# Kernel tuning notes

Hardware: AMD Instinct MI355X
Metric: run time of the kernel (lower is better)

The kernel has to match this reference:

```python
import jax, jax.numpy as jnp
import numpy as np

N_NODES = 100000
N_EDGES = 1200000
N_GRAPHS = 512
F_IN = 7
H = 64
N_CLASSES = 10


def _xavier(key, shape):
    fan_in, fan_out = shape[0], shape[1]
    limit = float(np.sqrt(6.0 / (fan_in + fan_out)))
    return jax.random.uniform(key, shape, jnp.float32, -limit, limit)


def setup_inputs() -> dict:
    key = jax.random.key(0)
    ks = jax.random.split(key, 16)
    x = jax.random.normal(ks[0], (N_NODES, F_IN), jnp.float32)
    edge_index = jax.random.randint(ks[1], (2, N_EDGES), 0, N_NODES, jnp.int64)
    batch = jnp.sort(jax.random.randint(ks[2], (N_NODES,), 0, N_GRAPHS, jnp.int64))
    d = {
        'x': x, 'edge_index': edge_index, 'batch': batch,
        'W_emb': _xavier(ks[3], (F_IN, H)), 'b_emb': jnp.zeros((H,), jnp.float32),
        'eps1': jnp.zeros((), jnp.float32),
        'W1a': _xavier(ks[4], (H, 2 * H)), 'b1a': jnp.zeros((2 * H,), jnp.float32),
        'W1b': _xavier(ks[5], (2 * H, H)), 'b1b': jnp.zeros((H,), jnp.float32),
        'eps2': jnp.zeros((), jnp.float32),
        'W2a': _xavier(ks[6], (H, 2 * H)), 'b2a': jnp.zeros((2 * H,), jnp.float32),
        'W2b': _xavier(ks[7], (2 * H, H)), 'b2b': jnp.zeros((H,), jnp.float32),
        'eps3': jnp.zeros((), jnp.float32),
        'W3a': _xavier(ks[8], (H, 2 * H)), 'b3a': jnp.zeros((2 * H,), jnp.float32),
        'W3b': _xavier(ks[9], (2 * H, H)), 'b3b': jnp.zeros((H,), jnp.float32),
        'Wc1': _xavier(ks[10], (2 * H, H)), 'bc1': jnp.zeros((H,), jnp.float32),
        'Wc2': _xavier(ks[11], (H, N_CLASSES)), 'bc2': jnp.zeros((N_CLASSES,), jnp.float32),
    }
    return d


def _gin_layer(x, eps, Wa, ba, Wb, bb, src, dst):
    # scatter-add aggregation of source features into destination nodes
    agg = jax.ops.segment_sum(x[src], dst, num_segments=N_NODES)
    h = (1.0 + eps) * x + agg
    h = jax.nn.relu(h @ Wa + ba) @ Wb + bb
    return jax.nn.elu(h)  # dropout is identity in eval mode


def reference(x, edge_index, batch,
              W_emb, b_emb,
              eps1, W1a, b1a, W1b, b1b,
              eps2, W2a, b2a, W2b, b2b,
              eps3, W3a, b3a, W3b, b3b,
              Wc1, bc1, Wc2, bc2):
    src, dst = edge_index[0], edge_index[1]
    h = x @ W_emb + b_emb                      # [N, H]
    h = _gin_layer(h, eps1, W1a, b1a, W1b, b1b, src, dst)
    h = _gin_layer(h, eps2, W2a, b2a, W2b, b2b, src, dst)
    h = _gin_layer(h, eps3, W3a, b3a, W3b, b3b, src, dst)
    # global mean + max pool per graph
    sums = jax.ops.segment_sum(h, batch, num_segments=N_GRAPHS)
    cnts = jax.ops.segment_sum(jnp.ones((h.shape[0], 1), h.dtype), batch, num_segments=N_GRAPHS)
    mean = sums / jnp.maximum(cnts, 1.0)
    mx = jax.ops.segment_max(h, batch, num_segments=N_GRAPHS)
    g = jnp.concatenate([mean, mx], axis=1)    # [G, 2H]
    out = jax.nn.relu(g @ Wc1 + bc1) @ Wc2 + bc2
    return out
```

## Files before the change

### kernel.cpp

```cpp
#include <hip/hip_runtime.h>
#include <hip/hip_bf16.h>
#include <math.h>

#define N_NODES 100000
#define N_EDGES 1200000
#define N_GRAPHS 512
#define NBUCKET 196
#define BSHIFT 9
#define TILE 2048
#define CSR_CAP 8192

typedef __bf16 bf16x8 __attribute__((ext_vector_type(8)));
typedef float f32x4 __attribute__((ext_vector_type(4)));

__device__ __forceinline__ unsigned f2ord(float f) {
  unsigned u = __float_as_uint(f);
  return (u & 0x80000000u) ? ~u : (u | 0x80000000u);
}
__device__ __forceinline__ float ord2f(unsigned u) {
  return (u & 0x80000000u) ? __uint_as_float(u & 0x7fffffffu) : __uint_as_float(~u);
}
__device__ __forceinline__ float bflo(unsigned u) { return __uint_as_float(u << 16); }
__device__ __forceinline__ float bfhi(unsigned u) { return __uint_as_float(u & 0xFFFF0000u); }

__global__ void bucket_hist_kernel(const int* __restrict__ dst, int* __restrict__ bcnt) {
  __shared__ int c[256];
  int t = threadIdx.x;
  c[t] = 0;
  __syncthreads();
  for (int e = blockIdx.x * 256 + t; e < N_EDGES; e += gridDim.x * 256)
    atomicAdd(&c[dst[e] >> BSHIFT], 1);
  __syncthreads();
  if (t < NBUCKET && c[t] > 0) atomicAdd(&bcnt[t], c[t]);
}

__global__ void bucket_scan_kernel(const int* __restrict__ bcnt,
                                   int* __restrict__ bbase,
                                   int* __restrict__ bcursor,
                                   int* __restrict__ rowp) {
  __shared__ int s[256];
  int t = threadIdx.x;
  int own = (t < NBUCKET) ? bcnt[t] : 0;
  s[t] = own;
  __syncthreads();
  for (int o = 1; o < 256; o <<= 1) {
    int v = (t >= o) ? s[t - o] : 0;
    __syncthreads();
    s[t] += v;
    __syncthreads();
  }
  if (t < NBUCKET) {
    int excl = s[t] - own;
    bbase[t] = excl;
    bcursor[t] = excl;
  }
  if (t == 0) {
    bbase[NBUCKET] = N_EDGES;
    rowp[N_NODES] = N_EDGES;
  }
}

__global__ void partition_kernel(const int* __restrict__ src, const int* __restrict__ dst,
                                 int* __restrict__ bcursor, unsigned* __restrict__ ent) {
  __shared__ int cnt[256];
  __shared__ int cnt2[256];
  __shared__ int lstart[256];
  __shared__ int gbase[256];
  __shared__ int s[256];
  __shared__ unsigned sorted[TILE];
  __shared__ unsigned char bid[TILE];
  int t = threadIdx.x;
  int e0 = blockIdx.x * TILE;
  cnt[t] = 0; cnt2[t] = 0;
  __syncthreads();

  unsigned v[8];
  int b[8];
#pragma unroll
  for (int u = 0; u < 8; ++u) {
    int e = e0 + u * 256 + t;
    b[u] = -1;
    if (e < N_EDGES) {
      int d = dst[e];
      b[u] = d >> BSHIFT;
      v[u] = (unsigned)src[e] | ((unsigned)(d & 511) << 17);
      atomicAdd(&cnt[b[u]], 1);
    }
  }
  __syncthreads();
  s[t] = cnt[t];
  __syncthreads();
  for (int o = 1; o < 256; o <<= 1) {
    int x = (t >= o) ? s[t - o] : 0;
    __syncthreads();
    s[t] += x;
    __syncthreads();
  }
  lstart[t] = s[t] - cnt[t];
  __syncthreads();
  if (t < NBUCKET) gbase[t] = (cnt[t] > 0) ? atomicAdd(&bcursor[t], cnt[t]) : 0;
  __syncthreads();
#pragma unroll
  for (int u = 0; u < 8; ++u) {
    if (b[u] >= 0) {
      int p = lstart[b[u]] + atomicAdd(&cnt2[b[u]], 1);
      sorted[p] = v[u];
      bid[p] = (unsigned char)b[u];
    }
  }
  __syncthreads();
  int ntile = min(TILE, N_EDGES - e0);
  for (int i = t; i < ntile; i += 256) {
    int bb = bid[i];
    ent[gbase[bb] + (i - lstart[bb])] = sorted[i];
  }
}

__launch_bounds__(256)
__global__ void bucket_csr_kernel(const unsigned* __restrict__ ent,
                                  const int* __restrict__ bbase,
                                  int* __restrict__ rowp,
                                  int* __restrict__ ssrc) {
  __shared__ unsigned le[CSR_CAP];
  __shared__ int deg[512];
  __shared__ int excl[512];
  __shared__ int ws[256];
  int t = threadIdx.x;
  int b = blockIdx.x;
  int base = bbase[b];
  int cntb = bbase[b + 1] - base;
  deg[t] = 0; deg[t + 256] = 0;
  __syncthreads();
  for (int i = t; i < cntb; i += 256) {
    unsigned e = ent[base + i];
    if (i < CSR_CAP) le[i] = e;
    atomicAdd(&deg[e >> 17], 1);
  }
  __syncthreads();
  int d0 = deg[t * 2], d1 = deg[t * 2 + 1];
  int sum2 = d0 + d1;
  ws[t] = sum2;
  __syncthreads();
  for (int o = 1; o < 256; o <<= 1) {
    int x = (t >= o) ? ws[t - o] : 0;
    __syncthreads();
    ws[t] += x;
    __syncthreads();
  }
  int run = ws[t] - sum2;
  excl[t * 2] = run; run += d0;
  excl[t * 2 + 1] = run;
  __syncthreads();
  int node0 = b << BSHIFT;
#pragma unroll
  for (int k = 0; k < 2; ++k) {
    int i = t * 2 + k;
    int n = node0 + i;
    if (n < N_NODES) rowp[n] = base + excl[i];
    deg[i] = excl[i];
  }
  __syncthreads();
  for (int i = t; i < cntb; i += 256) {
    unsigned e = (i < CSR_CAP) ? le[i] : ent[base + i];
    int p = atomicAdd(&deg[e >> 17], 1);
    ssrc[base + p] = (int)(e & 0x1FFFFu);
  }
}

__global__ void embed_kernel(const float* __restrict__ x,
                             const float* __restrict__ W,
                             const float* __restrict__ b,
                             __bf16* __restrict__ h) {
  __shared__ float Ws[7 * 64];
  __shared__ float bs[64];
  int t = threadIdx.x;
  for (int i = t; i < 7 * 64; i += 256) Ws[i] = W[i];
  if (t < 64) bs[t] = b[t];
  __syncthreads();
  int gid = blockIdx.x * 256 + t;
  int n = gid >> 6, f = gid & 63;
  const float* xr = x + n * 7;
  float acc = bs[f];
#pragma unroll
  for (int k = 0; k < 7; ++k) acc = fmaf(xr[k], Ws[k * 64 + f], acc);
  h[gid] = (__bf16)acc;
}

__global__ void convert_all_kernel(const float* __restrict__ W1a, const float* __restrict__ W1b,
                                   const float* __restrict__ W2a, const float* __restrict__ W2b,
                                   const float* __restrict__ W3a, const float* __restrict__ W3b,
                                   __bf16* __restrict__ wp,
                                   float* gsum, unsigned* gmax, int* gcnt) {
  int o = blockIdx.x * 256 + threadIdx.x;
  if (o < N_GRAPHS * 64) {
    gsum[o] = 0.0f;
    gmax[o] = 0x407FFFFFu;
  }
  if (o < N_GRAPHS) gcnt[o] = 0;
  int L = o >> 14, q = o & 16383;
  const float* Wa = (L == 0) ? W1a : (L == 1) ? W2a : W3a;
  const float* Wb = (L == 0) ? W1b : (L == 1) ? W2b : W3b;
  if (q < 8192) {
    int j = q & 7, c = (q >> 3) & 15, kc = (q >> 7) & 3, kt = (q >> 9) & 1, nt = q >> 10;
    wp[o] = (__bf16)Wa[(kt * 32 + kc * 8 + j) * 128 + nt * 16 + c];
  } else {
    int p = q - 8192;
    int j = p & 7, c = (p >> 3) & 15, kc = (p >> 7) & 3, kt = (p >> 9) & 3, nt2 = p >> 11;
    wp[o] = (__bf16)Wb[(kt * 32 + kc * 8 + j) * 64 + nt2 * 16 + c];
  }
}

__launch_bounds__(256)
__global__ void gin_fused4_kernel(const __bf16* __restrict__ hin,
                                  __bf16* __restrict__ hout,
                                  const int* __restrict__ row_ptr,
                                  const int* __restrict__ ssrc,
                                  const float* __restrict__ eps_p,
                                  const __bf16* __restrict__ W1p,
                                  const float* __restrict__ b1,
                                  const __bf16* __restrict__ W2p,
                                  const float* __restrict__ b2) {
  __shared__ __bf16 SM[4 * 2176];
  int t = threadIdx.x, lane = t & 63, wv = t >> 6;
  int c = lane & 15, kc = lane >> 4;
  int hl2 = (lane & 31) * 2;
  int par = lane >> 5;
  __bf16* AsW = &SM[wv * 2176];
  __bf16* HsW = AsW;
  float epsv = 1.0f + eps_p[0];
  int n0b = blockIdx.x * 64;
  int n0w = n0b + wv * 16;

  int rp = row_ptr[min(n0w + min(lane, 16), N_NODES)];

#define LD2(sidx) (*(const unsigned*)&hin[(size_t)(sidx) * 64 + hl2])

  for (int rr = 0; rr < 8; ++rr) {
    int rA = rr, rB = rr + 8;
    int nA = n0w + rA, nB = n0w + rB;
    int jA = __builtin_amdgcn_readfirstlane(__shfl(rp, rA));
    int eA = __builtin_amdgcn_readfirstlane(__shfl(rp, rA + 1));
    int jB = __builtin_amdgcn_readfirstlane(__shfl(rp, rB));
    int eB = __builtin_amdgcn_readfirstlane(__shfl(rp, rB + 1));
    float axA = 0.f, ayA = 0.f, axB = 0.f, ayB = 0.f;
    if (par == 0) {
      if (nA < N_NODES) { unsigned u = LD2(nA); axA = epsv * bflo(u); ayA = epsv * bfhi(u); }
      if (nB < N_NODES) { unsigned u = LD2(nB); axB = epsv * bflo(u); ayB = epsv * bfhi(u); }
    }
    while (jA + 8 <= eA && jB + 8 <= eB) {
      int a0 = ssrc[jA], a1 = ssrc[jA+1], a2 = ssrc[jA+2], a3 = ssrc[jA+3];
      int a4 = ssrc[jA+4], a5 = ssrc[jA+5], a6 = ssrc[jA+6], a7 = ssrc[jA+7];
      int b0 = ssrc[jB], b1_ = ssrc[jB+1], b2_ = ssrc[jB+2], b3_ = ssrc[jB+3];
      int b4 = ssrc[jB+4], b5 = ssrc[jB+5], b6 = ssrc[jB+6], b7 = ssrc[jB+7];
      unsigned uA0 = LD2(par ? a1 : a0), uA1 = LD2(par ? a3 : a2);
      unsigned uA2 = LD2(par ? a5 : a4), uA3 = LD2(par ? a7 : a6);
      unsigned uB0 = LD2(par ? b1_ : b0), uB1 = LD2(par ? b3_ : b2_);
      unsigned uB2 = LD2(par ? b5 : b4), uB3 = LD2(par ? b7 : b6);
      axA += (bflo(uA0) + bflo(uA1)) + (bflo(uA2) + bflo(uA3));
      ayA += (bfhi(uA0) + bfhi(uA1)) + (bfhi(uA2) + bfhi(uA3));
      axB += (bflo(uB0) + bflo(uB1)) + (bflo(uB2) + bflo(uB3));
      ayB += (bfhi(uB0) + bfhi(uB1)) + (bfhi(uB2) + bfhi(uB3));
      jA += 8; jB += 8;
    }
    while (jA + 8 <= eA) {
      int a0 = ssrc[jA], a1 = ssrc[jA+1], a2 = ssrc[jA+2], a3 = ssrc[jA+3];
      int a4 = ssrc[jA+4], a5 = ssrc[jA+5], a6 = ssrc[jA+6], a7 = ssrc[jA+7];
      unsigned u0 = LD2(par ? a1 : a0), u1 = LD2(par ? a3 : a2);
      unsigned u2 = LD2(par ? a5 : a4), u3 = LD2(par ? a7 : a6);
      axA += (bflo(u0) + bflo(u1)) + (bflo(u2) + bflo(u3));
      ayA += (bfhi(u0) + bfhi(u1)) + (bfhi(u2) + bfhi(u3));
      jA += 8;
    }
    if (jA + 4 <= eA) {
      int a0 = ssrc[jA], a1 = ssrc[jA+1], a2 = ssrc[jA+2], a3 = ssrc[jA+3];
      unsigned u0 = LD2(par ? a1 : a0), u1 = LD2(par ? a3 : a2);
      axA += bflo(u0) + bflo(u1);
      ayA += bfhi(u0) + bfhi(u1);
      jA += 4;
    }
    if (jA + 2 <= eA) {
      int a0 = ssrc[jA], a1 = ssrc[jA+1];
      unsigned u0 = LD2(par ? a1 : a0);
      axA += bflo(u0); ayA += bfhi(u0);
      jA += 2;
    }
    if (jA < eA && par == 0) {
      unsigned u0 = LD2(ssrc[jA]);
      axA += bflo(u0); ayA += bfhi(u0);
    }
    while (jB + 8 <= eB) {
      int b0 = ssrc[jB], b1_ = ssrc[jB+1], b2_ = ssrc[jB+2], b3_ = ssrc[jB+3];
      int b4 = ssrc[jB+4], b5 = ssrc[jB+5], b6 = ssrc[jB+6], b7 = ssrc[jB+7];
      unsigned u0 = LD2(par ? b1_ : b0), u1 = LD2(par ? b3_ : b2_);
      unsigned u2 = LD2(par ? b5 : b4), u3 = LD2(par ? b7 : b6);
      axB += (bflo(u0) + bflo(u1)) + (bflo(u2) + bflo(u3));
      ayB += (bfhi(u0) + bfhi(u1)) + (bfhi(u2) + bfhi(u3));
      jB += 8;
    }
    if (jB + 4 <= eB) {
      int b0 = ssrc[jB], b1_ = ssrc[jB+1], b2_ = ssrc[jB+2], b3_ = ssrc[jB+3];
      unsigned u0 = LD2(par ? b1_ : b0), u1 = LD2(par ? b3_ : b2_);
      axB += bflo(u0) + bflo(u1);
      ayB += bfhi(u0) + bfhi(u1);
      jB += 4;
    }
    if (jB + 2 <= eB) {
      int b0 = ssrc[jB], b1_ = ssrc[jB+1];
      unsigned u0 = LD2(par ? b1_ : b0);
      axB += bflo(u0); ayB += bfhi(u0);
      jB += 2;
    }
    if (jB < eB && par == 0) {
      unsigned u0 = LD2(ssrc[jB]);
      axB += bflo(u0); ayB += bfhi(u0);
    }
    axA += __shfl_xor(axA, 32); ayA += __shfl_xor(ayA, 32);
    axB += __shfl_xor(axB, 32); ayB += __shfl_xor(ayB, 32);
    if (par == 0) {
      union { __bf16 b[2]; unsigned u; } pA, pB;
      pA.b[0] = (__bf16)axA; pA.b[1] = (__bf16)ayA;
      pB.b[0] = (__bf16)axB; pB.b[1] = (__bf16)ayB;
      *(unsigned*)&AsW[rA * 72 + hl2] = pA.u;
      *(unsigned*)&AsW[rB * 72 + hl2] = pB.u;
    }
  }
#undef LD2

  bf16x8 a1_0 = *(const bf16x8*)&AsW[c * 72 + 0 * 32 + kc * 8];
  bf16x8 a1_1 = *(const bf16x8*)&AsW[c * 72 + 1 * 32 + kc * 8];
  f32x4 acc1[8];
#pragma unroll
  for (int nt = 0; nt < 8; ++nt) {
    float bv = b1[nt * 16 + c];
    f32x4 acc = {bv, bv, bv, bv};
    bf16x8 bf0 = *(const bf16x8*)&W1p[(nt * 2 + 0) * 512 + kc * 128 + c * 8];
    bf16x8 bf1 = *(const bf16x8*)&W1p[(nt * 2 + 1) * 512 + kc * 128 + c * 8];
    acc = __builtin_amdgcn_mfma_f32_16x16x32_bf16(a1_0, bf0, acc, 0, 0, 0);
    acc = __builtin_amdgcn_mfma_f32_16x16x32_bf16(a1_1, bf1, acc, 0, 0, 0);
    acc1[nt] = acc;
  }
#pragma unroll
  for (int nt = 0; nt < 8; ++nt) {
#pragma unroll
    for (int r = 0; r < 4; ++r) {
      HsW[(kc * 4 + r) * 136 + nt * 16 + c] = (__bf16)fmaxf(acc1[nt][r], 0.0f);
    }
  }

  bf16x8 a2[4];
#pragma unroll
  for (int kt = 0; kt < 4; ++kt)
    a2[kt] = *(const bf16x8*)&HsW[c * 136 + kt * 32 + kc * 8];
#pragma unroll
  for (int nt2 = 0; nt2 < 4; ++nt2) {
    float bv = b2[nt2 * 16 + c];
    f32x4 acc = {bv, bv, bv, bv};
#pragma unroll
    for (int kt = 0; kt < 4; ++kt) {
      bf16x8 bf = *(const bf16x8*)&W2p[(nt2 * 4 + kt) * 512 + kc * 128 + c * 8];
      acc = __builtin_amdgcn_mfma_f32_16x16x32_bf16(a2[kt], bf, acc, 0, 0, 0);
    }
#pragma unroll
    for (int r = 0; r < 4; ++r) {
      int g = n0b + wv * 16 + kc * 4 + r;
      if (g < N_NODES) {
        float o = acc[r];
        hout[(size_t)g * 64 + nt2 * 16 + c] = (__bf16)((o > 0.0f) ? o : expm1f(o));
      }
    }
  }
}

__global__ void pool_kernel(const __bf16* __restrict__ h,
                            const int* __restrict__ batch,
                            float* gsum, unsigned* gmax, int* gcnt) {
  int lane = threadIdx.x & 63;
  int wave = (blockIdx.x * blockDim.x + threadIdx.x) >> 6;
  int nwaves = (gridDim.x * blockDim.x) >> 6;
  int chunk = (N_NODES + nwaves - 1) / nwaves;
  int n0 = wave * chunk;
  int n1 = min(n0 + chunk, N_NODES);
  if (n0 >= N_NODES) return;
  int cur = batch[n0];
  float s = 0.0f, m = -2.0f;
  int cnt = 0;
  for (int n = n0; n < n1; ++n) {
    int g = batch[n];
    if (g != cur) {
      atomicAdd(&gsum[cur * 64 + lane], s);
      atomicMax(&gmax[cur * 64 + lane], f2ord(m));
      if (lane == 0) atomicAdd(&gcnt[cur], cnt);
      cur = g; s = 0.0f; m = -2.0f; cnt = 0;
    }
    float v = (float)h[(size_t)n * 64 + lane];
    s += v;
    m = fmaxf(m, v);
    ++cnt;
  }
  atomicAdd(&gsum[cur * 64 + lane], s);
  atomicMax(&gmax[cur * 64 + lane], f2ord(m));
  if (lane == 0) atomicAdd(&gcnt[cur], cnt);
}

__global__ void cls_kernel(const float* __restrict__ gsum,
                           const unsigned* __restrict__ gmax,
                           const int* __restrict__ gcnt,
                           const float* __restrict__ Wc1,
                           const float* __restrict__ bc1,
                           const float* __restrict__ Wc2,
                           const float* __restrict__ bc2,
                           float* __restrict__ out) {
  __shared__ float gv[128];
  __shared__ float tv[64];
  int g = blockIdx.x, l = threadIdx.x;
  float cnt = fmaxf((float)gcnt[g], 1.0f);
  gv[l] = gsum[g * 64 + l] / cnt;
  gv[64 + l] = ord2f(gmax[g * 64 + l]);
  __syncthreads();
  float acc = bc1[l];
#pragma unroll 8
  for (int k = 0; k < 128; ++k) acc = fmaf(gv[k], Wc1[k * 64 + l], acc);
  tv[l] = fmaxf(acc, 0.0f);
  __syncthreads();
  if (l < 10) {
    float o = bc2[l];
#pragma unroll
    for (int k = 0; k < 64; ++k) o = fmaf(tv[k], Wc2[k * 10 + l], o);
    out[g * 10 + l] = o;
  }
}

extern "C" void kernel_launch(void* const* d_in, const int* in_sizes, int n_in,
                              void* d_out, int out_size, void* d_ws, size_t ws_size,
                              hipStream_t stream) {
  const float* x     = (const float*)d_in[0];
  const int*   ei    = (const int*)d_in[1];
  const int*   batch = (const int*)d_in[2];
  const float* W_emb = (const float*)d_in[3];
  const float* b_emb = (const float*)d_in[4];
  const float* eps1  = (const float*)d_in[5];
  const float* W1a   = (const float*)d_in[6];
  const float* b1a   = (const float*)d_in[7];
  const float* W1b   = (const float*)d_in[8];
  const float* b1b   = (const float*)d_in[9];
  const float* eps2  = (const float*)d_in[10];
  const float* W2a   = (const float*)d_in[11];
  const float* b2a   = (const float*)d_in[12];
  const float* W2b   = (const float*)d_in[13];
  const float* b2b   = (const float*)d_in[14];
  const float* eps3  = (const float*)d_in[15];
  const float* W3a   = (const float*)d_in[16];
  const float* b3a   = (const float*)d_in[17];
  const float* W3b   = (const float*)d_in[18];
  const float* b3b   = (const float*)d_in[19];
  const float* Wc1   = (const float*)d_in[20];
  const float* bc1   = (const float*)d_in[21];
  const float* Wc2   = (const float*)d_in[22];
  const float* bc2   = (const float*)d_in[23];
  float* out = (float*)d_out;

  char* w = (char*)d_ws;
  __bf16*   h0   = (__bf16*)w;                     w += (size_t)N_NODES * 64 * 2;
  __bf16*   h1   = (__bf16*)w;                     w += (size_t)N_NODES * 64 * 2;
  float*    gsum = (float*)w;                      w += N_GRAPHS * 64 * 4;
  unsigned* gmax = (unsigned*)w;                   w += N_GRAPHS * 64 * 4;
  int*      gcnt = (int*)w;                        w += N_GRAPHS * 4;
  __bf16*   wp   = (__bf16*)w;                     w += 3 * 16384 * 2;
  int*      bcnt = (int*)w;                        w += 256 * 4;
  int*      bbase= (int*)w;                        w += 260 * 4;
  int*      bcur = (int*)w;                        w += 256 * 4;
  int*      rowp = (int*)w;                        w += (size_t)(N_NODES + 1) * 4;
  unsigned* ent  = (unsigned*)w;                   w += (size_t)N_EDGES * 4;
  int*      ssrc = (int*)w;                        w += (size_t)N_EDGES * 4;

  const int* src = ei;
  const int* dst = ei + N_EDGES;

  const float* epss[3] = {eps1, eps2, eps3};
  const float* bas[3]  = {b1a, b2a, b3a};
  const float* bbs[3]  = {b1b, b2b, b3b};

  hipMemsetAsync(bcnt, 0, 256 * sizeof(int), stream);
  bucket_hist_kernel<<<256, 256, 0, stream>>>(dst, bcnt);
  bucket_scan_kernel<<<1, 256, 0, stream>>>(bcnt, bbase, bcur, rowp);
  partition_kernel<<<(N_EDGES + TILE - 1) / TILE, 256, 0, stream>>>(src, dst, bcur, ent);
  bucket_csr_kernel<<<NBUCKET, 256, 0, stream>>>(ent, bbase, rowp, ssrc);

  convert_all_kernel<<<192, 256, 0, stream>>>(W1a, W1b, W2a, W2b, W3a, W3b, wp,
                                              gsum, gmax, gcnt);
  embed_kernel<<<(N_NODES * 64) / 256, 256, 0, stream>>>(x, W_emb, b_emb, h0);

  __bf16* hbuf[4] = {h0, h1, h0, h1};
  for (int L = 0; L < 3; ++L) {
    gin_fused4_kernel<<<(N_NODES + 63) / 64, 256, 0, stream>>>(
        hbuf[L], hbuf[L + 1], rowp, ssrc, epss[L],
        wp + (size_t)L * 16384, bas[L],
        wp + (size_t)L * 16384 + 8192, bbs[L]);
  }

  pool_kernel<<<512, 256, 0, stream>>>(h1, batch, gsum, gmax, gcnt);
  cls_kernel<<<N_GRAPHS, 64, 0, stream>>>(gsum, gmax, gcnt, Wc1, bc1, Wc2, bc2, out);
}
```

Baseline: 448.7 us.

## Fuse embedding into first GIN layer and restructure neighbor gather

```diff
diff --git a/kernel.cpp b/kernel.cpp
--- a/kernel.cpp
+++ b/kernel.cpp
@@ -20,8 +20,6 @@
 __device__ __forceinline__ float ord2f(unsigned u) {
   return (u & 0x80000000u) ? __uint_as_float(u & 0x7fffffffu) : __uint_as_float(~u);
 }
-__device__ __forceinline__ float bflo(unsigned u) { return __uint_as_float(u << 16); }
-__device__ __forceinline__ float bfhi(unsigned u) { return __uint_as_float(u & 0xFFFF0000u); }
 
 __global__ void bucket_hist_kernel(const int* __restrict__ dst, int* __restrict__ bcnt) {
   __shared__ int c[256];
@@ -167,25 +165,6 @@
   }
 }
 
-__global__ void embed_kernel(const float* __restrict__ x,
-                             const float* __restrict__ W,
-                             const float* __restrict__ b,
-                             __bf16* __restrict__ h) {
-  __shared__ float Ws[7 * 64];
-  __shared__ float bs[64];
-  int t = threadIdx.x;
-  for (int i = t; i < 7 * 64; i += 256) Ws[i] = W[i];
-  if (t < 64) bs[t] = b[t];
-  __syncthreads();
-  int gid = blockIdx.x * 256 + t;
-  int n = gid >> 6, f = gid & 63;
-  const float* xr = x + n * 7;
-  float acc = bs[f];
-#pragma unroll
-  for (int k = 0; k < 7; ++k) acc = fmaf(xr[k], Ws[k * 64 + f], acc);
-  h[gid] = (__bf16)acc;
-}
-
 __global__ void convert_all_kernel(const float* __restrict__ W1a, const float* __restrict__ W1b,
                                    const float* __restrict__ W2a, const float* __restrict__ W2b,
                                    const float* __restrict__ W3a, const float* __restrict__ W3b,
@@ -210,8 +189,122 @@
   }
 }
 
+__device__ __forceinline__ void mlp_tail(const __bf16* AsW, __bf16* HsW,
+                                         const __bf16* __restrict__ W1p,
+                                         const float* __restrict__ b1,
+                                         const __bf16* __restrict__ W2p,
+                                         const float* __restrict__ b2,
+                                         __bf16* __restrict__ hout,
+                                         int n0b, int wv, int c, int kc, int m0) {
+  bf16x8 a1_0 = *(const bf16x8*)&AsW[(m0 + c) * 72 + 0 * 32 + kc * 8];
+  bf16x8 a1_1 = *(const bf16x8*)&AsW[(m0 + c) * 72 + 1 * 32 + kc * 8];
+  f32x4 acc1[8];
+#pragma unroll
+  for (int nt = 0; nt < 8; ++nt) {
+    float bv = b1[nt * 16 + c];
+    f32x4 acc = {bv, bv, bv, bv};
+    bf16x8 bf0 = *(const bf16x8*)&W1p[(nt * 2 + 0) * 512 + kc * 128 + c * 8];
+    bf16x8 bf1 = *(const bf16x8*)&W1p[(nt * 2 + 1) * 512 + kc * 128 + c * 8];
+    acc = __builtin_amdgcn_mfma_f32_16x16x32_bf16(a1_0, bf0, acc, 0, 0, 0);
+    acc = __builtin_amdgcn_mfma_f32_16x16x32_bf16(a1_1, bf1, acc, 0, 0, 0);
+    acc1[nt] = acc;
+  }
+#pragma unroll
+  for (int nt = 0; nt < 8; ++nt) {
+#pragma unroll
+    for (int r = 0; r < 4; ++r) {
+      HsW[(m0 + kc * 4 + r) * 136 + nt * 16 + c] = (__bf16)fmaxf(acc1[nt][r], 0.0f);
+    }
+  }
+  bf16x8 a2[4];
+#pragma unroll
+  for (int kt = 0; kt < 4; ++kt)
+    a2[kt] = *(const bf16x8*)&HsW[(m0 + c) * 136 + kt * 32 + kc * 8];
+#pragma unroll
+  for (int nt2 = 0; nt2 < 4; ++nt2) {
+    float bv = b2[nt2 * 16 + c];
+    f32x4 acc = {bv, bv, bv, bv};
+#pragma unroll
+    for (int kt = 0; kt < 4; ++kt) {
+      bf16x8 bf = *(const bf16x8*)&W2p[(nt2 * 4 + kt) * 512 + kc * 128 + c * 8];
+      acc = __builtin_amdgcn_mfma_f32_16x16x32_bf16(a2[kt], bf, acc, 0, 0, 0);
+    }
+#pragma unroll
+    for (int r = 0; r < 4; ++r) {
+      int g = n0b + m0 + kc * 4 + r;
+      if (g < N_NODES) {
+        float o = acc[r];
+        hout[(size_t)g * 64 + nt2 * 16 + c] = (__bf16)((o > 0.0f) ? o : expm1f(o));
+      }
+    }
+  }
+}
+
 __launch_bounds__(256)
-__global__ void gin_fused4_kernel(const __bf16* __restrict__ hin,
+__global__ void gin_fused_l1_kernel(const float* __restrict__ x,
+                                    __bf16* __restrict__ hout,
+                                    const int* __restrict__ row_ptr,
+                                    const int* __restrict__ ssrc,
+                                    const float* __restrict__ eps_p,
+                                    const float* __restrict__ W_emb,
+                                    const float* __restrict__ b_emb,
+                                    const __bf16* __restrict__ W1p,
+                                    const float* __restrict__ b1,
+                                    const __bf16* __restrict__ W2p,
+                                    const float* __restrict__ b2) {
+  __shared__ __bf16 As[64 * 72];
+  __shared__ __bf16 Hs[64 * 136];
+  int t = threadIdx.x, lane = t & 63, wv = t >> 6;
+  int c = lane & 15, kc = lane >> 4;
+  int m0 = wv * 16;
+  float epsv = 1.0f + eps_p[0];
+  int n0b = blockIdx.x * 64;
+  int n0w = n0b + m0;
+
+  float w0 = W_emb[0 * 64 + lane], w1 = W_emb[1 * 64 + lane], w2 = W_emb[2 * 64 + lane];
+  float w3 = W_emb[3 * 64 + lane], w4 = W_emb[4 * 64 + lane], w5 = W_emb[5 * 64 + lane];
+  float w6 = W_emb[6 * 64 + lane];
+  float bl = b_emb[lane];
+
+  int rp = row_ptr[min(n0w + min(lane, 16), N_NODES)];
+
+#define EDGE7(sv, acc) { \
+    const float* xr = &x[(size_t)(sv) * 7]; \
+    acc = fmaf(xr[0], w0, acc); acc = fmaf(xr[1], w1, acc); \
+    acc = fmaf(xr[2], w2, acc); acc = fmaf(xr[3], w3, acc); \
+    acc = fmaf(xr[4], w4, acc); acc = fmaf(xr[5], w5, acc); \
+    acc = fmaf(xr[6], w6, acc); }
+
+  for (int r = 0; r < 16; ++r) {
+    int n = n0w + r;
+    float acc = 0.0f;
+    if (n < N_NODES) {
+      int j = __builtin_amdgcn_readfirstlane(__shfl(rp, r));
+      int e = __builtin_amdgcn_readfirstlane(__shfl(rp, r + 1));
+      acc = bl * (epsv + (float)(e - j));
+      const float* xn = &x[(size_t)n * 7];
+      float s0x = epsv * xn[0], s1x = epsv * xn[1], s2x = epsv * xn[2];
+      float s3x = epsv * xn[3], s4x = epsv * xn[4], s5x = epsv * xn[5];
+      float s6x = epsv * xn[6];
+      acc = fmaf(s0x, w0, acc); acc = fmaf(s1x, w1, acc); acc = fmaf(s2x, w2, acc);
+      acc = fmaf(s3x, w3, acc); acc = fmaf(s4x, w4, acc); acc = fmaf(s5x, w5, acc);
+      acc = fmaf(s6x, w6, acc);
+      for (; j + 2 <= e; j += 2) {
+        int sa = ssrc[j], sb = ssrc[j + 1];
+        EDGE7(sa, acc);
+        EDGE7(sb, acc);
+      }
+      if (j < e) { int sa = ssrc[j]; EDGE7(sa, acc); }
+    }
+    As[(m0 + r) * 72 + lane] = (__bf16)acc;
+  }
+#undef EDGE7
+
+  mlp_tail(As, Hs, W1p, b1, W2p, b2, hout, n0b, wv, c, kc, m0);
+}
+
+__launch_bounds__(256)
+__global__ void gin_fused5_kernel(const __bf16* __restrict__ hin,
                                   __bf16* __restrict__ hout,
                                   const int* __restrict__ row_ptr,
                                   const int* __restrict__ ssrc,
@@ -220,155 +313,82 @@
                                   const float* __restrict__ b1,
                                   const __bf16* __restrict__ W2p,
                                   const float* __restrict__ b2) {
-  __shared__ __bf16 SM[4 * 2176];
+  __shared__ __bf16 As[64 * 72];
+  __shared__ __bf16 Hs[64 * 136];
   int t = threadIdx.x, lane = t & 63, wv = t >> 6;
   int c = lane & 15, kc = lane >> 4;
-  int hl2 = (lane & 31) * 2;
-  int par = lane >> 5;
-  __bf16* AsW = &SM[wv * 2176];
-  __bf16* HsW = AsW;
+  int m0 = wv * 16;
   float epsv = 1.0f + eps_p[0];
   int n0b = blockIdx.x * 64;
-  int n0w = n0b + wv * 16;
+  int n0w = n0b + m0;
 
   int rp = row_ptr[min(n0w + min(lane, 16), N_NODES)];
 
-#define LD2(sidx) (*(const unsigned*)&hin[(size_t)(sidx) * 64 + hl2])
-
-  for (int rr = 0; rr < 8; ++rr) {
-    int rA = rr, rB = rr + 8;
-    int nA = n0w + rA, nB = n0w + rB;
-    int jA = __builtin_amdgcn_readfirstlane(__shfl(rp, rA));
-    int eA = __builtin_amdgcn_readfirstlane(__shfl(rp, rA + 1));
-    int jB = __builtin_amdgcn_readfirstlane(__shfl(rp, rB));
-    int eB = __builtin_amdgcn_readfirstlane(__shfl(rp, rB + 1));
-    float axA = 0.f, ayA = 0.f, axB = 0.f, ayB = 0.f;
-    if (par == 0) {
-      if (nA < N_NODES) { unsigned u = LD2(nA); axA = epsv * bflo(u); ayA = epsv * bfhi(u); }
-      if (nB < N_NODES) { unsigned u = LD2(nB); axB = epsv * bflo(u); ayB = epsv * bfhi(u); }
-    }
-    while (jA + 8 <= eA && jB + 8 <= eB) {
-      int a0 = ssrc[jA], a1 = ssrc[jA+1], a2 = ssrc[jA+2], a3 = ssrc[jA+3];
-      int a4 = ssrc[jA+4], a5 = ssrc[jA+5], a6 = ssrc[jA+6], a7 = ssrc[jA+7];
-      int b0 = ssrc[jB], b1_ = ssrc[jB+1], b2_ = ssrc[jB+2], b3_ = ssrc[jB+3];
-      int b4 = ssrc[jB+4], b5 = ssrc[jB+5], b6 = ssrc[jB+6], b7 = ssrc[jB+7];
-      unsigned uA0 = LD2(par ? a1 : a0), uA1 = LD2(par ? a3 : a2);
-      unsigned uA2 = LD2(par ? a5 : a4), uA3 = LD2(par ? a7 : a6);
-      unsigned uB0 = LD2(par ? b1_ : b0), uB1 = LD2(par ? b3_ : b2_);
-      unsigned uB2 = LD2(par ? b5 : b4), uB3 = LD2(par ? b7 : b6);
-      axA += (bflo(uA0) + bflo(uA1)) + (bflo(uA2) + bflo(uA3));
-      ayA += (bfhi(uA0) + bfhi(uA1)) + (bfhi(uA2) + bfhi(uA3));
-      axB += (bflo(uB0) + bflo(uB1)) + (bflo(uB2) + bflo(uB3));
-      ayB += (bfhi(uB0) + bfhi(uB1)) + (bfhi(uB2) + bfhi(uB3));
-      jA += 8; jB += 8;
-    }
-    while (jA + 8 <= eA) {
-      int a0 = ssrc[jA], a1 = ssrc[jA+1], a2 = ssrc[jA+2], a3 = ssrc[jA+3];
-      int a4 = ssrc[jA+4], a5 = ssrc[jA+5], a6 = ssrc[jA+6], a7 = ssrc[jA+7];
-      unsigned u0 = LD2(par ? a1 : a0), u1 = LD2(par ? a3 : a2);
-      unsigned u2 = LD2(par ? a5 : a4), u3 = LD2(par ? a7 : a6);
-      axA += (bflo(u0) + bflo(u1)) + (bflo(u2) + bflo(u3));
-      ayA += (bfhi(u0) + bfhi(u1)) + (bfhi(u2) + bfhi(u3));
-      jA += 8;
-    }
-    if (jA + 4 <= eA) {
-      int a0 = ssrc[jA], a1 = ssrc[jA+1], a2 = ssrc[jA+2], a3 = ssrc[jA+3];
-      unsigned u0 = LD2(par ? a1 : a0), u1 = LD2(par ? a3 : a2);
-      axA += bflo(u0) + bflo(u1);
-      ayA += bfhi(u0) + bfhi(u1);
-      jA += 4;
-    }
-    if (jA + 2 <= eA) {
-      int a0 = ssrc[jA], a1 = ssrc[jA+1];
-      unsigned u0 = LD2(par ? a1 : a0);
-      axA += bflo(u0); ayA += bfhi(u0);
-      jA += 2;
-    }
-    if (jA < eA && par == 0) {
-      unsigned u0 = LD2(ssrc[jA]);
-      axA += bflo(u0); ayA += bfhi(u0);
-    }
-    while (jB + 8 <= eB) {
-      int b0 = ssrc[jB], b1_ = ssrc[jB+1], b2_ = ssrc[jB+2], b3_ = ssrc[jB+3];
-      int b4 = ssrc[jB+4], b5 = ssrc[jB+5], b6 = ssrc[jB+6], b7 = ssrc[jB+7];
-      unsigned u0 = LD2(par ? b1_ : b0), u1 = LD2(par ? b3_ : b2_);
-      unsigned u2 = LD2(par ? b5 : b4), u3 = LD2(par ? b7 : b6);
-      axB += (bflo(u0) + bflo(u1)) + (bflo(u2) + bflo(u3));
-      ayB += (bfhi(u0) + bfhi(u1)) + (bfhi(u2) + bfhi(u3));
-      jB += 8;
-    }
-    if (jB + 4 <= eB) {
-      int b0 = ssrc[jB], b1_ = ssrc[jB+1], b2_ = ssrc[jB+2], b3_ = ssrc[jB+3];
-      unsigned u0 = LD2(par ? b1_ : b0), u1 = LD2(par ? b3_ : b2_);
-      axB += bflo(u0) + bflo(u1);
-      ayB += bfhi(u0) + bfhi(u1);
-      jB += 4;
-    }
-    if (jB + 2 <= eB) {
-      int b0 = ssrc[jB], b1_ = ssrc[jB+1];
-      unsigned u0 = LD2(par ? b1_ : b0);
-      axB += bflo(u0); ayB += bfhi(u0);
-      jB += 2;
-    }
-    if (jB < eB && par == 0) {
-      unsigned u0 = LD2(ssrc[jB]);
-      axB += bflo(u0); ayB += bfhi(u0);
-    }
-    axA += __shfl_xor(axA, 32); ayA += __shfl_xor(ayA, 32);
-    axB += __shfl_xor(axB, 32); ayB += __shfl_xor(ayB, 32);
-    if (par == 0) {
-      union { __bf16 b[2]; unsigned u; } pA, pB;
-      pA.b[0] = (__bf16)axA; pA.b[1] = (__bf16)ayA;
-      pB.b[0] = (__bf16)axB; pB.b[1] = (__bf16)ayB;
-      *(unsigned*)&AsW[rA * 72 + hl2] = pA.u;
-      *(unsigned*)&AsW[rB * 72 + hl2] = pB.u;
-    }
-  }
-#undef LD2
-
-  bf16x8 a1_0 = *(const bf16x8*)&AsW[c * 72 + 0 * 32 + kc * 8];
-  bf16x8 a1_1 = *(const bf16x8*)&AsW[c * 72 + 1 * 32 + kc * 8];
-  f32x4 acc1[8];
-#pragma unroll
-  for (int nt = 0; nt < 8; ++nt) {
-    float bv = b1[nt * 16 + c];
-    f32x4 acc = {bv, bv, bv, bv};
-    bf16x8 bf0 = *(const bf16x8*)&W1p[(nt * 2 + 0) * 512 + kc * 128 + c * 8];
-    bf16x8 bf1 = *(const bf16x8*)&W1p[(nt * 2 + 1) * 512 + kc * 128 + c * 8];
-    acc = __builtin_amdgcn_mfma_f32_16x16x32_bf16(a1_0, bf0, acc, 0, 0, 0);
-    acc = __builtin_amdgcn_mfma_f32_16x16x32_bf16(a1_1, bf1, acc, 0, 0, 0);
-    acc1[nt] = acc;
-  }
-#pragma unroll
-  for (int nt = 0; nt < 8; ++nt) {
-#pragma unroll
-    for (int r = 0; r < 4; ++r) {
-      HsW[(kc * 4 + r) * 136 + nt * 16 + c] = (__bf16)fmaxf(acc1[nt][r], 0.0f);
-    }
-  }
-
-  bf16x8 a2[4];
-#pragma unroll
-  for (int kt = 0; kt < 4; ++kt)
-    a2[kt] = *(const bf16x8*)&HsW[c * 136 + kt * 32 + kc * 8];
-#pragma unroll
-  for (int nt2 = 0; nt2 < 4; ++nt2) {
-    float bv = b2[nt2 * 16 + c];
-    f32x4 acc = {bv, bv, bv, bv};
-#pragma unroll
-    for (int kt = 0; kt < 4; ++kt) {
-      bf16x8 bf = *(const bf16x8*)&W2p[(nt2 * 4 + kt) * 512 + kc * 128 + c * 8];
-      acc = __builtin_amdgcn_mfma_f32_16x16x32_bf16(a2[kt], bf, acc, 0, 0, 0);
-    }
-#pragma unroll
-    for (int r = 0; r < 4; ++r) {
-      int g = n0b + wv * 16 + kc * 4 + r;
-      if (g < N_NODES) {
-        float o = acc[r];
-        hout[(size_t)g * 64 + nt2 * 16 + c] = (__bf16)((o > 0.0f) ? o : expm1f(o));
-      }
-    }
-  }
+#define DRAIN(j, e, acc) \
+  while (j + 4 <= e) { \
+    int q0 = ssrc[j], q1 = ssrc[j + 1], q2 = ssrc[j + 2], q3 = ssrc[j + 3]; \
+    float g0 = (float)hin[(size_t)q0 * 64 + lane]; \
+    float g1 = (float)hin[(size_t)q1 * 64 + lane]; \
+    float g2 = (float)hin[(size_t)q2 * 64 + lane]; \
+    float g3 = (float)hin[(size_t)q3 * 64 + lane]; \
+    acc += (g0 + g1) + (g2 + g3); j += 4; \
+  } \
+  for (; j < e; ++j) acc += (float)hin[(size_t)ssrc[j] * 64 + lane];
+
+  for (int rq = 0; rq < 4; ++rq) {
+    int r0 = rq, r1 = rq + 4, r2 = rq + 8, r3 = rq + 12;
+    int n0 = n0w + r0, n1 = n0w + r1, n2 = n0w + r2, n3 = n0w + r3;
+    int j0 = __builtin_amdgcn_readfirstlane(__shfl(rp, r0));
+    int e0 = __builtin_amdgcn_readfirstlane(__shfl(rp, r0 + 1));
+    int j1 = __builtin_amdgcn_readfirstlane(__shfl(rp, r1));
+    int e1 = __builtin_amdgcn_readfirstlane(__shfl(rp, r1 + 1));
+    int j2 = __builtin_amdgcn_readfirstlane(__shfl(rp, r2));
+    int e2 = __builtin_amdgcn_readfirstlane(__shfl(rp, r2 + 1));
+    int j3 = __builtin_amdgcn_readfirstlane(__shfl(rp, r3));
+    int e3 = __builtin_amdgcn_readfirstlane(__shfl(rp, r3 + 1));
+    float a0 = (n0 < N_NODES) ? epsv * (float)hin[(size_t)n0 * 64 + lane] : 0.0f;
+    float a1 = (n1 < N_NODES) ? epsv * (float)hin[(size_t)n1 * 64 + lane] : 0.0f;
+    float a2 = (n2 < N_NODES) ? epsv * (float)hin[(size_t)n2 * 64 + lane] : 0.0f;
+    float a3 = (n3 < N_NODES) ? epsv * (float)hin[(size_t)n3 * 64 + lane] : 0.0f;
+    while (j0 + 4 <= e0 && j1 + 4 <= e1 && j2 + 4 <= e2 && j3 + 4 <= e3) {
+      int s00 = ssrc[j0], s01 = ssrc[j0 + 1], s02 = ssrc[j0 + 2], s03 = ssrc[j0 + 3];
+      int s10 = ssrc[j1], s11 = ssrc[j1 + 1], s12 = ssrc[j1 + 2], s13 = ssrc[j1 + 3];
+      int s20 = ssrc[j2], s21 = ssrc[j2 + 1], s22 = ssrc[j2 + 2], s23 = ssrc[j2 + 3];
+      int s30 = ssrc[j3], s31 = ssrc[j3 + 1], s32 = ssrc[j3 + 2], s33 = ssrc[j3 + 3];
+      float f00 = (float)hin[(size_t)s00 * 64 + lane];
+      float f01 = (float)hin[(size_t)s01 * 64 + lane];
+      float f02 = (float)hin[(size_t)s02 * 64 + lane];
+      float f03 = (float)hin[(size_t)s03 * 64 + lane];
+      float f10 = (float)hin[(size_t)s10 * 64 + lane];
+      float f11 = (float)hin[(size_t)s11 * 64 + lane];
+      float f12 = (float)hin[(size_t)s12 * 64 + lane];
+      float f13 = (float)hin[(size_t)s13 * 64 + lane];
+      float f20 = (float)hin[(size_t)s20 * 64 + lane];
+      float f21 = (float)hin[(size_t)s21 * 64 + lane];
+      float f22 = (float)hin[(size_t)s22 * 64 + lane];
+      float f23 = (float)hin[(size_t)s23 * 64 + lane];
+      float f30 = (float)hin[(size_t)s30 * 64 + lane];
+      float f31 = (float)hin[(size_t)s31 * 64 + lane];
+      float f32_ = (float)hin[(size_t)s32 * 64 + lane];
+      float f33 = (float)hin[(size_t)s33 * 64 + lane];
+      a0 += (f00 + f01) + (f02 + f03);
+      a1 += (f10 + f11) + (f12 + f13);
+      a2 += (f20 + f21) + (f22 + f23);
+      a3 += (f30 + f31) + (f32_ + f33);
+      j0 += 4; j1 += 4; j2 += 4; j3 += 4;
+    }
+    DRAIN(j0, e0, a0);
+    DRAIN(j1, e1, a1);
+    DRAIN(j2, e2, a2);
+    DRAIN(j3, e3, a3);
+    As[(m0 + r0) * 72 + lane] = (__bf16)a0;
+    As[(m0 + r1) * 72 + lane] = (__bf16)a1;
+    As[(m0 + r2) * 72 + lane] = (__bf16)a2;
+    As[(m0 + r3) * 72 + lane] = (__bf16)a3;
+  }
+#undef DRAIN
+
+  mlp_tail(As, Hs, W1p, b1, W2p, b2, hout, n0b, wv, c, kc, m0);
 }
 
 __global__ void pool_kernel(const __bf16* __restrict__ h,
@@ -476,10 +496,6 @@
   const int* src = ei;
   const int* dst = ei + N_EDGES;
 
-  const float* epss[3] = {eps1, eps2, eps3};
-  const float* bas[3]  = {b1a, b2a, b3a};
-  const float* bbs[3]  = {b1b, b2b, b3b};
-
   hipMemsetAsync(bcnt, 0, 256 * sizeof(int), stream);
   bucket_hist_kernel<<<256, 256, 0, stream>>>(dst, bcnt);
   bucket_scan_kernel<<<1, 256, 0, stream>>>(bcnt, bbase, bcur, rowp);
@@ -488,16 +504,18 @@
 
   convert_all_kernel<<<192, 256, 0, stream>>>(W1a, W1b, W2a, W2b, W3a, W3b, wp,
                                               gsum, gmax, gcnt);
-  embed_kernel<<<(N_NODES * 64) / 256, 256, 0, stream>>>(x, W_emb, b_emb, h0);
-
-  __bf16* hbuf[4] = {h0, h1, h0, h1};
-  for (int L = 0; L < 3; ++L) {
-    gin_fused4_kernel<<<(N_NODES + 63) / 64, 256, 0, stream>>>(
-        hbuf[L], hbuf[L + 1], rowp, ssrc, epss[L],
-        wp + (size_t)L * 16384, bas[L],
-        wp + (size_t)L * 16384 + 8192, bbs[L]);
-  }
-
-  pool_kernel<<<512, 256, 0, stream>>>(h1, batch, gsum, gmax, gcnt);
+
+  const int NGB = (N_NODES + 63) / 64;
+  gin_fused_l1_kernel<<<NGB, 256, 0, stream>>>(
+      x, h0, rowp, ssrc, eps1, W_emb, b_emb,
+      wp + 0 * 16384, b1a, wp + 0 * 16384 + 8192, b1b);
+  gin_fused5_kernel<<<NGB, 256, 0, stream>>>(
+      h0, h1, rowp, ssrc, eps2,
+      wp + 1 * 16384, b2a, wp + 1 * 16384 + 8192, b2b);
+  gin_fused5_kernel<<<NGB, 256, 0, stream>>>(
+      h1, h0, rowp, ssrc, eps3,
+      wp + 2 * 16384, b3a, wp + 2 * 16384 + 8192, b3b);
+
+  pool_kernel<<<512, 256, 0, stream>>>(h0, batch, gsum, gmax, gcnt);
   cls_kernel<<<N_GRAPHS, 64, 0, stream>>>(gsum, gmax, gcnt, Wc1, bc1, Wc2, bc2, out);
 }
```

New measurement: 446.6 us. About the same (-0.5%).

## Aggregate neighbors per wave-tile via packed edges and LDS float atomics

Applied to the files above, without the earlier changes.

```diff
diff --git a/kernel.cpp b/kernel.cpp
--- a/kernel.cpp
+++ b/kernel.cpp
@@ -20,8 +20,6 @@
 __device__ __forceinline__ float ord2f(unsigned u) {
   return (u & 0x80000000u) ? __uint_as_float(u & 0x7fffffffu) : __uint_as_float(~u);
 }
-__device__ __forceinline__ float bflo(unsigned u) { return __uint_as_float(u << 16); }
-__device__ __forceinline__ float bfhi(unsigned u) { return __uint_as_float(u & 0xFFFF0000u); }
 
 __global__ void bucket_hist_kernel(const int* __restrict__ dst, int* __restrict__ bcnt) {
   __shared__ int c[256];
@@ -120,7 +118,7 @@
 __global__ void bucket_csr_kernel(const unsigned* __restrict__ ent,
                                   const int* __restrict__ bbase,
                                   int* __restrict__ rowp,
-                                  int* __restrict__ ssrc) {
+                                  unsigned* __restrict__ epack) {
   __shared__ unsigned le[CSR_CAP];
   __shared__ int deg[512];
   __shared__ int excl[512];
@@ -163,7 +161,7 @@
   for (int i = t; i < cntb; i += 256) {
     unsigned e = (i < CSR_CAP) ? le[i] : ent[base + i];
     int p = atomicAdd(&deg[e >> 17], 1);
-    ssrc[base + p] = (int)(e & 0x1FFFFu);
+    epack[base + p] = (e & 0x1FFFFu) | (((e >> 17) & 63u) << 17);
   }
 }
 
@@ -211,123 +209,77 @@
 }
 
 __launch_bounds__(256)
-__global__ void gin_fused4_kernel(const __bf16* __restrict__ hin,
+__global__ void gin_fused6_kernel(const __bf16* __restrict__ hin,
                                   __bf16* __restrict__ hout,
                                   const int* __restrict__ row_ptr,
-                                  const int* __restrict__ ssrc,
+                                  const unsigned* __restrict__ epack,
                                   const float* __restrict__ eps_p,
                                   const __bf16* __restrict__ W1p,
                                   const float* __restrict__ b1,
                                   const __bf16* __restrict__ W2p,
                                   const float* __restrict__ b2) {
-  __shared__ __bf16 SM[4 * 2176];
+  __shared__ float Ag[64 * 68];
+  __bf16* Hs = (__bf16*)Ag;
   int t = threadIdx.x, lane = t & 63, wv = t >> 6;
   int c = lane & 15, kc = lane >> 4;
-  int hl2 = (lane & 31) * 2;
-  int par = lane >> 5;
-  __bf16* AsW = &SM[wv * 2176];
-  __bf16* HsW = AsW;
+  int m0 = wv * 16;
   float epsv = 1.0f + eps_p[0];
   int n0b = blockIdx.x * 64;
-  int n0w = n0b + wv * 16;
-
-  int rp = row_ptr[min(n0w + min(lane, 16), N_NODES)];
-
-#define LD2(sidx) (*(const unsigned*)&hin[(size_t)(sidx) * 64 + hl2])
-
-  for (int rr = 0; rr < 8; ++rr) {
-    int rA = rr, rB = rr + 8;
-    int nA = n0w + rA, nB = n0w + rB;
-    int jA = __builtin_amdgcn_readfirstlane(__shfl(rp, rA));
-    int eA = __builtin_amdgcn_readfirstlane(__shfl(rp, rA + 1));
-    int jB = __builtin_amdgcn_readfirstlane(__shfl(rp, rB));
-    int eB = __builtin_amdgcn_readfirstlane(__shfl(rp, rB + 1));
-    float axA = 0.f, ayA = 0.f, axB = 0.f, ayB = 0.f;
-    if (par == 0) {
-      if (nA < N_NODES) { unsigned u = LD2(nA); axA = epsv * bflo(u); ayA = epsv * bfhi(u); }
-      if (nB < N_NODES) { unsigned u = LD2(nB); axB = epsv * bflo(u); ayB = epsv * bfhi(u); }
-    }
-    while (jA + 8 <= eA && jB + 8 <= eB) {
-      int a0 = ssrc[jA], a1 = ssrc[jA+1], a2 = ssrc[jA+2], a3 = ssrc[jA+3];
-      int a4 = ssrc[jA+4], a5 = ssrc[jA+5], a6 = ssrc[jA+6], a7 = ssrc[jA+7];
-      int b0 = ssrc[jB], b1_ = ssrc[jB+1], b2_ = ssrc[jB+2], b3_ = ssrc[jB+3];
-      int b4 = ssrc[jB+4], b5 = ssrc[jB+5], b6 = ssrc[jB+6], b7 = ssrc[jB+7];
-      unsigned uA0 = LD2(par ? a1 : a0), uA1 = LD2(par ? a3 : a2);
-      unsigned uA2 = LD2(par ? a5 : a4), uA3 = LD2(par ? a7 : a6);
-      unsigned uB0 = LD2(par ? b1_ : b0), uB1 = LD2(par ? b3_ : b2_);
-      unsigned uB2 = LD2(par ? b5 : b4), uB3 = LD2(par ? b7 : b6);
-      axA += (bflo(uA0) + bflo(uA1)) + (bflo(uA2) + bflo(uA3));
-      ayA += (bfhi(uA0) + bfhi(uA1)) + (bfhi(uA2) + bfhi(uA3));
-      axB += (bflo(uB0) + bflo(uB1)) + (bflo(uB2) + bflo(uB3));
-      ayB += (bfhi(uB0) + bfhi(uB1)) + (bfhi(uB2) + bfhi(uB3));
-      jA += 8; jB += 8;
-    }
-    while (jA + 8 <= eA) {
-      int a0 = ssrc[jA], a1 = ssrc[jA+1], a2 = ssrc[jA+2], a3 = ssrc[jA+3];
-      int a4 = ssrc[jA+4], a5 = ssrc[jA+5], a6 = ssrc[jA+6], a7 = ssrc[jA+7];
-      unsigned u0 = LD2(par ? a1 : a0), u1 = LD2(par ? a3 : a2);
-      unsigned u2 = LD2(par ? a5 : a4), u3 = LD2(par ? a7 : a6);
-      axA += (bflo(u0) + bflo(u1)) + (bflo(u2) + bflo(u3));
-      ayA += (bfhi(u0) + bfhi(u1)) + (bfhi(u2) + bfhi(u3));
-      jA += 8;
-    }
-    if (jA + 4 <= eA) {
-      int a0 = ssrc[jA], a1 = ssrc[jA+1], a2 = ssrc[jA+2], a3 = ssrc[jA+3];
-      unsigned u0 = LD2(par ? a1 : a0), u1 = LD2(par ? a3 : a2);
-      axA += bflo(u0) + bflo(u1);
-      ayA += bfhi(u0) + bfhi(u1);
-      jA += 4;
-    }
-    if (jA + 2 <= eA) {
-      int a0 = ssrc[jA], a1 = ssrc[jA+1];
-      unsigned u0 = LD2(par ? a1 : a0);
-      axA += bflo(u0); ayA += bfhi(u0);
-      jA += 2;
-    }
-    if (jA < eA && par == 0) {
-      unsigned u0 = LD2(ssrc[jA]);
-      axA += bflo(u0); ayA += bfhi(u0);
-    }
-    while (jB + 8 <= eB) {
-      int b0 = ssrc[jB], b1_ = ssrc[jB+1], b2_ = ssrc[jB+2], b3_ = ssrc[jB+3];
-      int b4 = ssrc[jB+4], b5 = ssrc[jB+5], b6 = ssrc[jB+6], b7 = ssrc[jB+7];
-      unsigned u0 = LD2(par ? b1_ : b0), u1 = LD2(par ? b3_ : b2_);
-      unsigned u2 = LD2(par ? b5 : b4), u3 = LD2(par ? b7 : b6);
-      axB += (bflo(u0) + bflo(u1)) + (bflo(u2) + bflo(u3));
-      ayB += (bfhi(u0) + bfhi(u1)) + (bfhi(u2) + bfhi(u3));
-      jB += 8;
-    }
-    if (jB + 4 <= eB) {
-      int b0 = ssrc[jB], b1_ = ssrc[jB+1], b2_ = ssrc[jB+2], b3_ = ssrc[jB+3];
-      unsigned u0 = LD2(par ? b1_ : b0), u1 = LD2(par ? b3_ : b2_);
-      axB += bflo(u0) + bflo(u1);
-      ayB += bfhi(u0) + bfhi(u1);
-      jB += 4;
-    }
-    if (jB + 2 <= eB) {
-      int b0 = ssrc[jB], b1_ = ssrc[jB+1];
-      unsigned u0 = LD2(par ? b1_ : b0);
-      axB += bflo(u0); ayB += bfhi(u0);
-      jB += 2;
-    }
-    if (jB < eB && par == 0) {
-      unsigned u0 = LD2(ssrc[jB]);
-      axB += bflo(u0); ayB += bfhi(u0);
-    }
-    axA += __shfl_xor(axA, 32); ayA += __shfl_xor(ayA, 32);
-    axB += __shfl_xor(axB, 32); ayB += __shfl_xor(ayB, 32);
-    if (par == 0) {
-      union { __bf16 b[2]; unsigned u; } pA, pB;
-      pA.b[0] = (__bf16)axA; pA.b[1] = (__bf16)ayA;
-      pB.b[0] = (__bf16)axB; pB.b[1] = (__bf16)ayB;
-      *(unsigned*)&AsW[rA * 72 + hl2] = pA.u;
-      *(unsigned*)&AsW[rB * 72 + hl2] = pB.u;
-    }
-  }
-#undef LD2
-
-  bf16x8 a1_0 = *(const bf16x8*)&AsW[c * 72 + 0 * 32 + kc * 8];
-  bf16x8 a1_1 = *(const bf16x8*)&AsW[c * 72 + 1 * 32 + kc * 8];
+  int n0w = n0b + m0;
+
+#pragma unroll
+  for (int r = 0; r < 16; ++r) {
+    int n = n0w + r;
+    float v = (n < N_NODES) ? epsv * (float)hin[(size_t)n * 64 + lane] : 0.0f;
+    Ag[(m0 + r) * 68 + lane] = v;
+  }
+
+  int rs = __builtin_amdgcn_readfirstlane(row_ptr[min(n0w, N_NODES)]);
+  int re = __builtin_amdgcn_readfirstlane(row_ptr[min(n0w + 16, N_NODES)]);
+
+  int k = rs;
+  while (k + 16 <= re) {
+    unsigned ev[16];
+#pragma unroll
+    for (int i = 0; i < 16; ++i) ev[i] = epack[k + i];
+    float fv[16];
+#pragma unroll
+    for (int i = 0; i < 16; ++i)
+      fv[i] = (float)hin[(size_t)(ev[i] & 0x1FFFFu) * 64 + lane];
+#pragma unroll
+    for (int i = 0; i < 16; ++i)
+      atomicAdd(&Ag[(ev[i] >> 17) * 68 + lane], fv[i]);
+    k += 16;
+  }
+  while (k + 4 <= re) {
+    unsigned ev[4];
+#pragma unroll
+    for (int i = 0; i < 4; ++i) ev[i] = epack[k + i];
+    float fv[4];
+#pragma unroll
+    for (int i = 0; i < 4; ++i)
+      fv[i] = (float)hin[(size_t)(ev[i] & 0x1FFFFu) * 64 + lane];
+#pragma unroll
+    for (int i = 0; i < 4; ++i)
+      atomicAdd(&Ag[(ev[i] >> 17) * 68 + lane], fv[i]);
+    k += 4;
+  }
+  for (; k < re; ++k) {
+    unsigned e = epack[k];
+    float f = (float)hin[(size_t)(e & 0x1FFFFu) * 64 + lane];
+    atomicAdd(&Ag[(e >> 17) * 68 + lane], f);
+  }
+
+  bf16x8 a1_0, a1_1;
+  {
+    const float* rowa = &Ag[(m0 + c) * 68];
+#pragma unroll
+    for (int i = 0; i < 8; ++i) {
+      a1_0[i] = (__bf16)rowa[kc * 8 + i];
+      a1_1[i] = (__bf16)rowa[32 + kc * 8 + i];
+    }
+  }
+
   f32x4 acc1[8];
 #pragma unroll
   for (int nt = 0; nt < 8; ++nt) {
@@ -343,14 +295,14 @@
   for (int nt = 0; nt < 8; ++nt) {
 #pragma unroll
     for (int r = 0; r < 4; ++r) {
-      HsW[(kc * 4 + r) * 136 + nt * 16 + c] = (__bf16)fmaxf(acc1[nt][r], 0.0f);
+      Hs[(m0 + kc * 4 + r) * 136 + nt * 16 + c] = (__bf16)fmaxf(acc1[nt][r], 0.0f);
     }
   }
 
   bf16x8 a2[4];
 #pragma unroll
   for (int kt = 0; kt < 4; ++kt)
-    a2[kt] = *(const bf16x8*)&HsW[c * 136 + kt * 32 + kc * 8];
+    a2[kt] = *(const bf16x8*)&Hs[(m0 + c) * 136 + kt * 32 + kc * 8];
 #pragma unroll
   for (int nt2 = 0; nt2 < 4; ++nt2) {
     float bv = b2[nt2 * 16 + c];
@@ -362,7 +314,7 @@
     }
 #pragma unroll
     for (int r = 0; r < 4; ++r) {
-      int g = n0b + wv * 16 + kc * 4 + r;
+      int g = n0b + m0 + kc * 4 + r;
       if (g < N_NODES) {
         float o = acc[r];
         hout[(size_t)g * 64 + nt2 * 16 + c] = (__bf16)((o > 0.0f) ? o : expm1f(o));
@@ -471,7 +423,7 @@
   int*      bcur = (int*)w;                        w += 256 * 4;
   int*      rowp = (int*)w;                        w += (size_t)(N_NODES + 1) * 4;
   unsigned* ent  = (unsigned*)w;                   w += (size_t)N_EDGES * 4;
-  int*      ssrc = (int*)w;                        w += (size_t)N_EDGES * 4;
+  unsigned* epk  = (unsigned*)w;                   w += (size_t)N_EDGES * 4;
 
   const int* src = ei;
   const int* dst = ei + N_EDGES;
@@ -484,16 +436,17 @@
   bucket_hist_kernel<<<256, 256, 0, stream>>>(dst, bcnt);
   bucket_scan_kernel<<<1, 256, 0, stream>>>(bcnt, bbase, bcur, rowp);
   partition_kernel<<<(N_EDGES + TILE - 1) / TILE, 256, 0, stream>>>(src, dst, bcur, ent);
-  bucket_csr_kernel<<<NBUCKET, 256, 0, stream>>>(ent, bbase, rowp, ssrc);
+  bucket_csr_kernel<<<NBUCKET, 256, 0, stream>>>(ent, bbase, rowp, epk);
 
   convert_all_kernel<<<192, 256, 0, stream>>>(W1a, W1b, W2a, W2b, W3a, W3b, wp,
                                               gsum, gmax, gcnt);
   embed_kernel<<<(N_NODES * 64) / 256, 256, 0, stream>>>(x, W_emb, b_emb, h0);
 
+  const int NGB = (N_NODES + 63) / 64;
   __bf16* hbuf[4] = {h0, h1, h0, h1};
   for (int L = 0; L < 3; ++L) {
-    gin_fused4_kernel<<<(N_NODES + 63) / 64, 256, 0, stream>>>(
-        hbuf[L], hbuf[L + 1], rowp, ssrc, epss[L],
+    gin_fused6_kernel<<<NGB, 256, 0, stream>>>(
+        hbuf[L], hbuf[L + 1], rowp, epk, epss[L],
         wp + (size_t)L * 16384, bas[L],
         wp + (size_t)L * 16384 + 8192, bbs[L]);
   }
```

After: 1.567 ms. 249% more time.
